# Performance work log

Hardware: AMD Instinct MI355X
Metric: run time of the kernel (lower is better)

The kernel has to match this reference:

```python
import jax, jax.numpy as jnp
import numpy as np

FEATURE_DIM = 768
NUM_HEADS = 16
HEAD_DIM = FEATURE_DIM // NUM_HEADS
SCALE = HEAD_DIM ** -0.5


def setup_inputs() -> dict:
    key = jax.random.key(0)
    ks = jax.random.split(key, 9)
    B, N, C = 4, 2048, FEATURE_DIM
    s = 0.02
    return {
        "x": jax.random.normal(ks[0], (B, N, C), dtype=jnp.float32),
        "wq": jax.random.normal(ks[1], (C, C), dtype=jnp.float32) * s,
        "bq": jax.random.normal(ks[2], (C,), dtype=jnp.float32) * s,
        "wk": jax.random.normal(ks[3], (C, C), dtype=jnp.float32) * s,
        "bk": jax.random.normal(ks[4], (C,), dtype=jnp.float32) * s,
        "wv": jax.random.normal(ks[5], (C, C), dtype=jnp.float32) * s,
        "bv": jax.random.normal(ks[6], (C,), dtype=jnp.float32) * s,
        "wo": jax.random.normal(ks[7], (C, C), dtype=jnp.float32) * s,
        "bo": jax.random.normal(ks[8], (C,), dtype=jnp.float32) * s,
    }


def reference(x, wq, bq, wk, bk, wv, bv, wo, bo):
    B, N, C = x.shape
    H, D = NUM_HEADS, HEAD_DIM
    # Linear layers use weight of shape (out, in): y = x @ W.T + b
    def proj(w, b):
        return (jnp.einsum("bnc,dc->bnd", x, w) + b).reshape(B, N, H, D).transpose(0, 2, 1, 3)
    q = proj(wq, bq)  # [B,H,N,D]
    k = proj(wk, bk)
    v = proj(wv, bv)
    attn = jnp.einsum("bhnd,bhmd->bhnm", q, k) * SCALE
    attn = jax.nn.softmax(attn, axis=-1)  # dropout = identity (eval mode)
    y = jnp.einsum("bhnm,bhmd->bhnd", attn, v).transpose(0, 2, 1, 3).reshape(B, N, C)
    y = y + x
    out = jnp.einsum("bnc,dc->bnd", y, wo) + bo
    out = out + y
    return out + x
```

## Files before the change

kernel.cpp:

```cpp
#include <hip/hip_runtime.h>
#include <hip/hip_bf16.h>

#define B_ 4
#define N_ 2048
#define C_ 768
#define H_ 16
#define D_ 48
#define SCALE_ 0.14433756729740643f
#define LOG2E_ 1.44269504088896f

using bf16 = __hip_bfloat16;
using bf16x8 = __attribute__((ext_vector_type(8))) short;
using f32x4  = __attribute__((ext_vector_type(4))) float;
using f32x16 = __attribute__((ext_vector_type(16))) float;

__device__ __forceinline__ unsigned short f2b(float f) {
  bf16 h = __float2bfloat16(f);
  return *reinterpret_cast<unsigned short*>(&h);
}
__device__ __forceinline__ unsigned int pack2(float lo, float hi) {
  return (unsigned int)f2b(lo) | ((unsigned int)f2b(hi) << 16);
}
__device__ __forceinline__ uint4 ld8f_cvt(const float* p) {
  float4 a = *reinterpret_cast<const float4*>(p);
  float4 b = *reinterpret_cast<const float4*>(p + 4);
  uint4 u;
  u.x = pack2(a.x, a.y); u.y = pack2(a.z, a.w);
  u.z = pack2(b.x, b.y); u.w = pack2(b.z, b.w);
  return u;
}
__device__ __forceinline__ void gload_lds16(const bf16* g, bf16* l) {
  __builtin_amdgcn_global_load_lds(
      (const __attribute__((address_space(1))) unsigned int*)g,
      (__attribute__((address_space(3))) unsigned int*)l, 16, 0, 0);
}

__global__ __launch_bounds__(256) void cvt_bf16(
    const float* __restrict__ x,  const float* __restrict__ wq,
    const float* __restrict__ wk, const float* __restrict__ wv,
    const float* __restrict__ wo,
    bf16* __restrict__ xb, bf16* __restrict__ wqkvb, bf16* __restrict__ wob)
{
  const int job = blockIdx.y;
  const float* src; bf16* dst; int n;
  if (job == 0)      { src = x;  dst = xb;              n = B_ * N_ * C_; }
  else if (job == 1) { src = wq; dst = wqkvb;           n = C_ * C_; }
  else if (job == 2) { src = wk; dst = wqkvb + C_ * C_; n = C_ * C_; }
  else if (job == 3) { src = wv; dst = wqkvb + 2 * C_ * C_; n = C_ * C_; }
  else               { src = wo; dst = wob;             n = C_ * C_; }
  const int stride = gridDim.x * 256 * 8;
  for (int i = (blockIdx.x * 256 + threadIdx.x) * 8; i < n; i += stride)
    *(uint4*)(dst + i) = ld8f_cvt(src + i);
}

__global__ __launch_bounds__(256) void gemm_qkv(
    const bf16* __restrict__ A, const bf16* __restrict__ Bw,
    const float* __restrict__ bq, const float* __restrict__ bk,
    const float* __restrict__ bv,
    bf16* __restrict__ Q, bf16* __restrict__ K, bf16* __restrict__ V)
{
  __shared__ __align__(16) bf16 As[128 * 64];
  __shared__ __align__(16) bf16 Bs[128 * 64];

  const int tid  = threadIdx.x;
  const int lane = tid & 63, wid = tid >> 6;
  const int wm = (wid >> 1) * 64, wn = (wid & 1) * 64;
  const int row0 = blockIdx.y * 128, col0 = blockIdx.x * 128;
  const int mb = lane & 15, g4 = lane >> 4;
  const int srow = lane >> 3;
  const int schunk = (lane & 7) ^ (srow & 7);

  f32x4 acc[4][4];
#pragma unroll
  for (int i = 0; i < 4; ++i)
#pragma unroll
    for (int j = 0; j < 4; ++j) acc[i][j] = (f32x4){0.f, 0.f, 0.f, 0.f};

  for (int k0 = 0; k0 < C_; k0 += 64) {
#pragma unroll
    for (int t = 0; t < 4; ++t) {
      const int rt = wid * 32 + t * 8;
      gload_lds16(A  + (size_t)(row0 + rt + srow) * C_ + k0 + schunk * 8,
                  As + rt * 64);
      gload_lds16(Bw + (size_t)(col0 + rt + srow) * C_ + k0 + schunk * 8,
                  Bs + rt * 64);
    }
    __syncthreads();
#pragma unroll
    for (int ks = 0; ks < 2; ++ks) {
      const int kchunk = ks * 4 + g4;
      bf16x8 af[4], bfr[4];
#pragma unroll
      for (int i = 0; i < 4; ++i) {
        const int row = wm + i * 16 + mb;
        af[i] = *(const bf16x8*)(As + row * 64 + (kchunk ^ (row & 7)) * 8);
      }
#pragma unroll
      for (int j = 0; j < 4; ++j) {
        const int col = wn + j * 16 + mb;
        bfr[j] = *(const bf16x8*)(Bs + col * 64 + (kchunk ^ (col & 7)) * 8);
      }
#pragma unroll
      for (int i = 0; i < 4; ++i)
#pragma unroll
        for (int j = 0; j < 4; ++j)
          acc[i][j] = __builtin_amdgcn_mfma_f32_16x16x32_bf16(af[i], bfr[j], acc[i][j], 0, 0, 0);
    }
    __syncthreads();
  }

  const int z = blockIdx.x / 6;
  const float* bias = (z == 0) ? bq : (z == 1) ? bk : bv;
  bf16* dst = (z == 0) ? Q : (z == 1) ? K : V;
  const float sc = (z == 0) ? (SCALE_ * LOG2E_) : 1.0f;
  const int crow = g4 * 4;
#pragma unroll
  for (int j = 0; j < 4; ++j) {
    const int oo = col0 - z * 768 + wn + j * 16 + mb;
    const int h = oo / D_, d = oo % D_;
    const float bb = bias[oo];
#pragma unroll
    for (int i = 0; i < 4; ++i) {
#pragma unroll
      for (int reg = 0; reg < 4; ++reg) {
        const int r = row0 + wm + i * 16 + crow + reg;
        const int b_ = r >> 11, n = r & (N_ - 1);
        dst[(((size_t)(b_ * H_ + h)) * N_ + n) * D_ + d] =
            __float2bfloat16((acc[i][j][reg] + bb) * sc);
      }
    }
  }
}

__global__ __launch_bounds__(256) void qkv_reshape(
    bf16* __restrict__ Q, bf16* __restrict__ K, bf16* __restrict__ V)
{
  __shared__ short T[64 * 50];
  const int bh = blockIdx.x;
  const int t0 = blockIdx.y * 64;
  const int tid = threadIdx.x;
  const size_t base = (size_t)bh * (N_ * D_) + (size_t)t0 * D_;
  bf16* bufs[3] = {Q, K, V};
#pragma unroll 1
  for (int wbuf = 0; wbuf < 3; ++wbuf) {
    bf16* P = bufs[wbuf] + base;
    for (int cc = tid; cc < 384; cc += 256) {
      const int r = cc / 6, ch = cc % 6;
      bf16x8 v8 = *(const bf16x8*)(P + r * D_ + ch * 8);
#pragma unroll
      for (int e = 0; e < 8; ++e) T[r * 50 + ch * 8 + e] = v8[e];
    }
    __syncthreads();
    if (wbuf < 2) {
      for (int w = tid; w < 384; w += 256) {
        const int sub = w / 192, rem = w % 192;
        const int kc = rem / 64, rem2 = rem % 64;
        const int g2 = rem2 >> 5, m5 = rem2 & 31;
        bf16x8 o;
#pragma unroll
        for (int e = 0; e < 8; ++e)
          o[e] = T[(sub * 32 + m5) * 50 + kc * 16 + g2 * 8 + e];
        *(bf16x8*)(P + w * 8) = o;
      }
    } else {
      for (int w = tid; w < 384; w += 256) {
        const int df = w / 128, rem = w % 128;
        const int hf = rem / 64, rem2 = rem % 64;
        const int g4 = rem2 >> 4, cx = rem2 & 15;
        bf16x8 o;
#pragma unroll
        for (int e = 0; e < 8; ++e)
          o[e] = T[(hf * 32 + g4 * 8 + e) * 50 + df * 16 + cx];
        *(bf16x8*)(P + w * 8) = o;
      }
    }
    __syncthreads();
  }
}

__global__ __launch_bounds__(256) void attn_mfma(
    const bf16* __restrict__ Qf, const bf16* __restrict__ Kf,
    const bf16* __restrict__ Vf, const float* __restrict__ x,
    bf16* __restrict__ Yb)
{
  __shared__ __align__(16) bf16 Ps[4 * 32 * 72];

  const int tid  = threadIdx.x;
  const int lane = tid & 63, wid = tid >> 6;
  const int m5 = lane & 31;
  const int g4 = lane >> 4, c = lane & 15;
  const int bh = blockIdx.x;
  const int b_ = bh >> 4, h = bh & 15;
  const int q0 = blockIdx.y * 128 + wid * 32;
  const size_t slab = (size_t)bh * (N_ * D_);
  bf16* Pw = Ps + wid * (32 * 72);

  bf16x8 qf[3];
  const int kgq = q0 >> 5;
#pragma unroll
  for (int kc = 0; kc < 3; ++kc)
    qf[kc] = *(const bf16x8*)(Qf + slab + (size_t)(((kgq * 3 + kc) * 64) + lane) * 8);

  const short one_bf = (short)0x3F80;
  const bf16x8 onesf = {one_bf, one_bf, one_bf, one_bf,
                        one_bf, one_bf, one_bf, one_bf};

  f32x4 Oacc[2][3];
  f32x4 Lacc[2];
#pragma unroll
  for (int s = 0; s < 2; ++s) {
    Lacc[s] = (f32x4){0.f, 0.f, 0.f, 0.f};
#pragma unroll
    for (int df = 0; df < 3; ++df) Oacc[s][df] = (f32x4){0.f, 0.f, 0.f, 0.f};
  }

  bf16x8 kf[2][2][3];
  auto loadK = [&](int kk0, int p) {
    const int kg = kk0 >> 5;
#pragma unroll
    for (int mt = 0; mt < 2; ++mt)
#pragma unroll
      for (int kc = 0; kc < 3; ++kc)
        kf[p][mt][kc] = *(const bf16x8*)(Kf + slab +
            (size_t)((((kg + mt) * 3 + kc) * 64) + lane) * 8);
  };
  auto body = [&](int k0c, int p) {
    const int kt = k0c >> 6;
    bf16x8 vf[3][2];
#pragma unroll
    for (int df = 0; df < 3; ++df)
#pragma unroll
      for (int hf = 0; hf < 2; ++hf)
        vf[df][hf] = *(const bf16x8*)(Vf + slab +
            (size_t)((((kt * 3 + df) * 2 + hf) * 64) + lane) * 8);
    f32x16 st[2];
#pragma unroll
    for (int mt = 0; mt < 2; ++mt) {
      f32x16 z;
#pragma unroll
      for (int r = 0; r < 16; ++r) z[r] = 0.f;
      st[mt] = __builtin_amdgcn_mfma_f32_32x32x16_bf16(kf[p][mt][0], qf[0], z, 0, 0, 0);
      st[mt] = __builtin_amdgcn_mfma_f32_32x32x16_bf16(kf[p][mt][1], qf[1], st[mt], 0, 0, 0);
      st[mt] = __builtin_amdgcn_mfma_f32_32x32x16_bf16(kf[p][mt][2], qf[2], st[mt], 0, 0, 0);
    }
#pragma unroll
    for (int mt = 0; mt < 2; ++mt)
#pragma unroll
      for (int r = 0; r < 16; ++r)
        st[mt][r] = __builtin_amdgcn_exp2f(st[mt][r]);
#pragma unroll
    for (int mt = 0; mt < 2; ++mt)
#pragma unroll
      for (int q = 0; q < 4; ++q) {
        uint2 w;
        w.x = pack2(st[mt][4 * q + 0], st[mt][4 * q + 1]);
        w.y = pack2(st[mt][4 * q + 2], st[mt][4 * q + 3]);
        *(uint2*)(Pw + m5 * 72 + mt * 32 + 8 * q + 4 * (lane >> 5)) = w;
      }
#pragma unroll
    for (int s = 0; s < 2; ++s) {
      bf16x8 pf[2];
#pragma unroll
      for (int hf = 0; hf < 2; ++hf)
        pf[hf] = *(const bf16x8*)(Pw + (s * 16 + c) * 72 + hf * 32 + 8 * g4);
#pragma unroll
      for (int df = 0; df < 3; ++df) {
        Oacc[s][df] = __builtin_amdgcn_mfma_f32_16x16x32_bf16(pf[0], vf[df][0], Oacc[s][df], 0, 0, 0);
        Oacc[s][df] = __builtin_amdgcn_mfma_f32_16x16x32_bf16(pf[1], vf[df][1], Oacc[s][df], 0, 0, 0);
      }
      Lacc[s] = __builtin_amdgcn_mfma_f32_16x16x32_bf16(pf[0], onesf, Lacc[s], 0, 0, 0);
      Lacc[s] = __builtin_amdgcn_mfma_f32_16x16x32_bf16(pf[1], onesf, Lacc[s], 0, 0, 0);
    }
  };

  loadK(0, 0);
  for (int k0 = 0; k0 < N_; k0 += 128) {
    loadK(k0 + 64, 1);
    body(k0, 0);
    if (k0 + 128 < N_) loadK(k0 + 128, 0);
    body(k0 + 64, 1);
  }

#pragma unroll
  for (int s = 0; s < 2; ++s) {
#pragma unroll
    for (int r = 0; r < 4; ++r) {
      const float inv = 1.f / Lacc[s][r];
      const int n = q0 + s * 16 + 4 * g4 + r;
      const size_t off = ((size_t)(b_ * N_ + n)) * C_ + h * D_ + c;
#pragma unroll
      for (int df = 0; df < 3; ++df)
        Yb[off + df * 16] =
            __float2bfloat16(Oacc[s][df][r] * inv + x[off + df * 16]);
    }
  }
}

__global__ __launch_bounds__(256) void gemm_out(
    const bf16* __restrict__ Yb, const bf16* __restrict__ Bw,
    const float* __restrict__ bo, const float* __restrict__ x,
    float* __restrict__ out)
{
  __shared__ __align__(16) bf16 As[128 * 64];
  __shared__ __align__(16) bf16 Bs[128 * 64];

  const int tid  = threadIdx.x;
  const int lane = tid & 63, wid = tid >> 6;
  const int wm = (wid >> 1) * 64, wn = (wid & 1) * 64;
  const int row0 = blockIdx.y * 128, col0 = blockIdx.x * 128;
  const int mb = lane & 15, g4 = lane >> 4;
  const int srow = lane >> 3;
  const int schunk = (lane & 7) ^ (srow & 7);

  f32x4 acc[4][4];
#pragma unroll
  for (int i = 0; i < 4; ++i)
#pragma unroll
    for (int j = 0; j < 4; ++j) acc[i][j] = (f32x4){0.f, 0.f, 0.f, 0.f};

  for (int k0 = 0; k0 < C_; k0 += 64) {
#pragma unroll
    for (int t = 0; t < 4; ++t) {
      const int rt = wid * 32 + t * 8;
      gload_lds16(Yb + (size_t)(row0 + rt + srow) * C_ + k0 + schunk * 8,
                  As + rt * 64);
      gload_lds16(Bw + (size_t)(col0 + rt + srow) * C_ + k0 + schunk * 8,
                  Bs + rt * 64);
    }
    __syncthreads();
#pragma unroll
    for (int ks = 0; ks < 2; ++ks) {
      const int kchunk = ks * 4 + g4;
      bf16x8 af[4], bfr[4];
#pragma unroll
      for (int i = 0; i < 4; ++i) {
        const int row = wm + i * 16 + mb;
        af[i] = *(const bf16x8*)(As + row * 64 + (kchunk ^ (row & 7)) * 8);
      }
#pragma unroll
      for (int j = 0; j < 4; ++j) {
        const int col = wn + j * 16 + mb;
        bfr[j] = *(const bf16x8*)(Bs + col * 64 + (kchunk ^ (col & 7)) * 8);
      }
#pragma unroll
      for (int i = 0; i < 4; ++i)
#pragma unroll
        for (int j = 0; j < 4; ++j)
          acc[i][j] = __builtin_amdgcn_mfma_f32_16x16x32_bf16(af[i], bfr[j], acc[i][j], 0, 0, 0);
    }
    __syncthreads();
  }

  const int crow = g4 * 4;
#pragma unroll
  for (int j = 0; j < 4; ++j) {
    const int o = col0 + wn + j * 16 + mb;
    const float bb = bo[o];
#pragma unroll
    for (int i = 0; i < 4; ++i) {
#pragma unroll
      for (int reg = 0; reg < 4; ++reg) {
        const int r = row0 + wm + i * 16 + crow + reg;
        const size_t off = (size_t)r * C_ + o;
        out[off] = acc[i][j][reg] + bb + __bfloat162float(Yb[off]) + x[off];
      }
    }
  }
}

extern "C" void kernel_launch(void* const* d_in, const int* in_sizes, int n_in,
                              void* d_out, int out_size, void* d_ws, size_t ws_size,
                              hipStream_t stream)
{
  const float* x  = (const float*)d_in[0];
  const float* wq = (const float*)d_in[1];
  const float* bq = (const float*)d_in[2];
  const float* wk = (const float*)d_in[3];
  const float* bk = (const float*)d_in[4];
  const float* wv = (const float*)d_in[5];
  const float* bv = (const float*)d_in[6];
  const float* wo = (const float*)d_in[7];
  const float* bo = (const float*)d_in[8];
  float* out = (float*)d_out;

  const size_t nEl = (size_t)B_ * N_ * C_;
  const size_t wEl = (size_t)C_ * C_;
  bf16* Q     = (bf16*)d_ws;
  bf16* K     = Q + nEl;
  bf16* V     = K + nEl;
  bf16* Yb    = V + nEl;
  bf16* xb    = Yb + nEl;
  bf16* wqkvb = xb + nEl;
  bf16* wob   = wqkvb + 3 * wEl;

  dim3 gcvt(768, 5);
  cvt_bf16<<<gcvt, dim3(256), 0, stream>>>(x, wq, wk, wv, wo, xb, wqkvb, wob);

  dim3 gqkv(18, 64);
  gemm_qkv<<<gqkv, dim3(256), 0, stream>>>(xb, wqkvb, bq, bk, bv, Q, K, V);

  dim3 grs(B_ * H_, N_ / 64);
  qkv_reshape<<<grs, dim3(256), 0, stream>>>(Q, K, V);

  dim3 gattn(B_ * H_, N_ / 128);
  attn_mfma<<<gattn, dim3(256), 0, stream>>>(Q, K, V, x, Yb);

  dim3 gout(6, 64);
  gemm_out<<<gout, dim3(256), 0, stream>>>(Yb, wob, bo, x, out);
}
```

Before: 272.0 us.

## Fuse QKV reshape into GEMM epilogue and software-pipeline attention loop

The separate qkv_reshape kernel is removed. The QKV GEMM now stages its output tile in shared memory and writes Q/K/V directly in the MFMA-fragment layout the attention kernel expects, which saves one kernel launch and a full read/write pass over Q, K and V. The attention loop is restructured so the QK^T/exp for tile t overlaps with the PV product for tile t-1, using double-buffered P tiles in LDS. A packed bf16 convert builtin is also used when available. The cost is doubled LDS for P and extra syncs in the GEMM epilogue.

Measured after the change: 297.2 us. 1.09x slower.

```diff
diff --git a/kernel.cpp b/kernel.cpp
--- a/kernel.cpp
+++ b/kernel.cpp
@@ -14,12 +14,24 @@
 using f32x4  = __attribute__((ext_vector_type(4))) float;
 using f32x16 = __attribute__((ext_vector_type(16))) float;
 
+#if defined(__has_builtin)
+#if __has_builtin(__builtin_amdgcn_cvt_pk_bf16_f32)
+#define HAS_PK_BF16 1
+#endif
+#endif
+
 __device__ __forceinline__ unsigned short f2b(float f) {
   bf16 h = __float2bfloat16(f);
   return *reinterpret_cast<unsigned short*>(&h);
 }
 __device__ __forceinline__ unsigned int pack2(float lo, float hi) {
+#ifdef HAS_PK_BF16
+  typedef __bf16 bf16x2v __attribute__((ext_vector_type(2)));
+  bf16x2v r = __builtin_amdgcn_cvt_pk_bf16_f32(lo, hi);
+  union { bf16x2v v; unsigned int u; } cv; cv.v = r; return cv.u;
+#else
   return (unsigned int)f2b(lo) | ((unsigned int)f2b(hi) << 16);
+#endif
 }
 __device__ __forceinline__ uint4 ld8f_cvt(const float* p) {
   float4 a = *reinterpret_cast<const float4*>(p);
@@ -59,8 +71,9 @@
     const float* __restrict__ bv,
     bf16* __restrict__ Q, bf16* __restrict__ K, bf16* __restrict__ V)
 {
-  __shared__ __align__(16) bf16 As[128 * 64];
-  __shared__ __align__(16) bf16 Bs[128 * 64];
+  __shared__ __align__(16) bf16 SH[2 * 128 * 64];
+  bf16* As = SH;
+  bf16* Bs = SH + 128 * 64;
 
   const int tid  = threadIdx.x;
   const int lane = tid & 63, wid = tid >> 6;
@@ -113,68 +126,75 @@
   const float* bias = (z == 0) ? bq : (z == 1) ? bk : bv;
   bf16* dst = (z == 0) ? Q : (z == 1) ? K : V;
   const float sc = (z == 0) ? (SCALE_ * LOG2E_) : 1.0f;
-  const int crow = g4 * 4;
-#pragma unroll
-  for (int j = 0; j < 4; ++j) {
-    const int oo = col0 - z * 768 + wn + j * 16 + mb;
-    const int h = oo / D_, d = oo % D_;
-    const float bb = bias[oo];
-#pragma unroll
-    for (int i = 0; i < 4; ++i) {
-#pragma unroll
-      for (int reg = 0; reg < 4; ++reg) {
-        const int r = row0 + wm + i * 16 + crow + reg;
-        const int b_ = r >> 11, n = r & (N_ - 1);
-        dst[(((size_t)(b_ * H_ + h)) * N_ + n) * D_ + d] =
-            __float2bfloat16((acc[i][j][reg] + bb) * sc);
-      }
-    }
-  }
-}
-
-__global__ __launch_bounds__(256) void qkv_reshape(
-    bf16* __restrict__ Q, bf16* __restrict__ K, bf16* __restrict__ V)
-{
-  __shared__ short T[64 * 50];
-  const int bh = blockIdx.x;
-  const int t0 = blockIdx.y * 64;
-  const int tid = threadIdx.x;
-  const size_t base = (size_t)bh * (N_ * D_) + (size_t)t0 * D_;
-  bf16* bufs[3] = {Q, K, V};
+  const int obase = (blockIdx.x % 6) * 128;
+  bf16* Cs = SH;
+
 #pragma unroll 1
-  for (int wbuf = 0; wbuf < 3; ++wbuf) {
-    bf16* P = bufs[wbuf] + base;
-    for (int cc = tid; cc < 384; cc += 256) {
-      const int r = cc / 6, ch = cc % 6;
-      bf16x8 v8 = *(const bf16x8*)(P + r * D_ + ch * 8);
-#pragma unroll
-      for (int e = 0; e < 8; ++e) T[r * 50 + ch * 8 + e] = v8[e];
-    }
-    __syncthreads();
-    if (wbuf < 2) {
-      for (int w = tid; w < 384; w += 256) {
-        const int sub = w / 192, rem = w % 192;
-        const int kc = rem / 64, rem2 = rem % 64;
-        const int g2 = rem2 >> 5, m5 = rem2 & 31;
-        bf16x8 o;
-#pragma unroll
-        for (int e = 0; e < 8; ++e)
-          o[e] = T[(sub * 32 + m5) * 50 + kc * 16 + g2 * 8 + e];
-        *(bf16x8*)(P + w * 8) = o;
+  for (int h2 = 0; h2 < 2; ++h2) {
+    __syncthreads();
+    if ((wid >> 1) == h2) {
+      if (z < 2) {
+#pragma unroll
+        for (int j = 0; j < 4; ++j) {
+          const int col = wn + j * 16 + mb;
+          const float bb = bias[obase + col];
+#pragma unroll
+          for (int i = 0; i < 4; ++i)
+#pragma unroll
+            for (int reg = 0; reg < 4; ++reg) {
+              const int rowL = i * 16 + 4 * g4 + reg;
+              Cs[rowL * 136 + col] =
+                  __float2bfloat16((acc[i][j][reg] + bb) * sc);
+            }
+        }
+      } else {
+#pragma unroll
+        for (int j = 0; j < 4; ++j) {
+          const int col = wn + j * 16 + mb;
+          const float bb = bias[obase + col];
+#pragma unroll
+          for (int i = 0; i < 4; ++i) {
+            uint2 wv;
+            wv.x = pack2(acc[i][j][0] + bb, acc[i][j][1] + bb);
+            wv.y = pack2(acc[i][j][2] + bb, acc[i][j][3] + bb);
+            *(uint2*)(Cs + col * 72 + i * 16 + 4 * g4) = wv;
+          }
+        }
+      }
+    }
+    __syncthreads();
+    const int rbase = row0 + h2 * 64;
+    const int bb_ = rbase >> 11;
+    const int nbase = rbase & (N_ - 1);
+    if (z < 2) {
+#pragma unroll
+      for (int t = 0; t < 4; ++t) {
+        const int w = t * 256 + tid;
+        const int m5w = w & 31, obw = (w >> 5) & 15, kgL = w >> 9;
+        const int m = (obase >> 3) + obw;
+        const int hh = m / 6, dd8 = m % 6;
+        const int n = nbase + kgL * 32 + m5w;
+        const size_t slab = (size_t)(bb_ * H_ + hh) * (N_ * D_);
+        const size_t chunk = (size_t)(((n >> 5) * 3 + (dd8 >> 1)) * 64
+                                      + (dd8 & 1) * 32 + m5w);
+        *(bf16x8*)(dst + slab + chunk * 8) =
+            *(const bf16x8*)(Cs + (kgL * 32 + m5w) * 136 + obw * 8);
       }
     } else {
-      for (int w = tid; w < 384; w += 256) {
-        const int df = w / 128, rem = w % 128;
-        const int hf = rem / 64, rem2 = rem % 64;
-        const int g4 = rem2 >> 4, cx = rem2 & 15;
-        bf16x8 o;
-#pragma unroll
-        for (int e = 0; e < 8; ++e)
-          o[e] = T[(hf * 32 + g4 * 8 + e) * 50 + df * 16 + cx];
-        *(bf16x8*)(P + w * 8) = o;
-      }
-    }
-    __syncthreads();
+#pragma unroll
+      for (int t = 0; t < 4; ++t) {
+        const int w = t * 256 + tid;
+        const int cw = w & 15, cb = (w >> 4) & 7, g4w = (w >> 7) & 3, hfw = w >> 9;
+        const int o = obase + cb * 16 + cw;
+        const int hh = o / 48, df = (o % 48) >> 4;
+        const int kt = nbase >> 6;
+        const size_t slab = (size_t)(bb_ * H_ + hh) * (N_ * D_);
+        const size_t chunk = (size_t)(((kt * 3 + df) * 2 + hfw) * 64
+                                      + g4w * 16 + cw);
+        *(bf16x8*)(dst + slab + chunk * 8) =
+            *(const bf16x8*)(Cs + (cb * 16 + cw) * 72 + hfw * 32 + g4w * 8);
+      }
+    }
   }
 }
 
@@ -183,23 +203,24 @@
     const bf16* __restrict__ Vf, const float* __restrict__ x,
     bf16* __restrict__ Yb)
 {
-  __shared__ __align__(16) bf16 Ps[4 * 32 * 72];
+  __shared__ __align__(16) bf16 Ps[4 * 2 * 32 * 72];
 
   const int tid  = threadIdx.x;
   const int lane = tid & 63, wid = tid >> 6;
-  const int m5 = lane & 31;
+  const int m5 = lane & 31, g2h = lane >> 5;
   const int g4 = lane >> 4, c = lane & 15;
   const int bh = blockIdx.x;
   const int b_ = bh >> 4, h = bh & 15;
   const int q0 = blockIdx.y * 128 + wid * 32;
   const size_t slab = (size_t)bh * (N_ * D_);
-  bf16* Pw = Ps + wid * (32 * 72);
+  bf16* Pw0 = Ps + wid * 2 * (32 * 72);
+  bf16* Pw1 = Pw0 + 32 * 72;
 
   bf16x8 qf[3];
   const int kgq = q0 >> 5;
 #pragma unroll
   for (int kc = 0; kc < 3; ++kc)
-    qf[kc] = *(const bf16x8*)(Qf + slab + (size_t)(((kgq * 3 + kc) * 64) + lane) * 8);
+    qf[kc] = *(const bf16x8*)(Qf + slab + (size_t)((kgq * 3 + kc) * 64 + lane) * 8);
 
   const short one_bf = (short)0x3F80;
   const bf16x8 onesf = {one_bf, one_bf, one_bf, one_bf,
@@ -215,54 +236,51 @@
   }
 
   bf16x8 kf[2][2][3];
-  auto loadK = [&](int kk0, int p) {
-    const int kg = kk0 >> 5;
+  bf16x8 vf[3][2];
+
+  auto loadK = [&](int t, int p) {
 #pragma unroll
     for (int mt = 0; mt < 2; ++mt)
 #pragma unroll
       for (int kc = 0; kc < 3; ++kc)
         kf[p][mt][kc] = *(const bf16x8*)(Kf + slab +
-            (size_t)((((kg + mt) * 3 + kc) * 64) + lane) * 8);
+            (size_t)(((2 * t + mt) * 3 + kc) * 64 + lane) * 8);
   };
-  auto body = [&](int k0c, int p) {
-    const int kt = k0c >> 6;
-    bf16x8 vf[3][2];
+  auto loadV = [&](int t) {
 #pragma unroll
     for (int df = 0; df < 3; ++df)
 #pragma unroll
       for (int hf = 0; hf < 2; ++hf)
         vf[df][hf] = *(const bf16x8*)(Vf + slab +
-            (size_t)((((kt * 3 + df) * 2 + hf) * 64) + lane) * 8);
-    f32x16 st[2];
+            (size_t)(((t * 3 + df) * 2 + hf) * 64 + lane) * 8);
+  };
+  auto SexpPack = [&](int p, bf16* pw) {
 #pragma unroll
     for (int mt = 0; mt < 2; ++mt) {
-      f32x16 z;
-#pragma unroll
-      for (int r = 0; r < 16; ++r) z[r] = 0.f;
-      st[mt] = __builtin_amdgcn_mfma_f32_32x32x16_bf16(kf[p][mt][0], qf[0], z, 0, 0, 0);
-      st[mt] = __builtin_amdgcn_mfma_f32_32x32x16_bf16(kf[p][mt][1], qf[1], st[mt], 0, 0, 0);
-      st[mt] = __builtin_amdgcn_mfma_f32_32x32x16_bf16(kf[p][mt][2], qf[2], st[mt], 0, 0, 0);
-    }
-#pragma unroll
-    for (int mt = 0; mt < 2; ++mt)
-#pragma unroll
-      for (int r = 0; r < 16; ++r)
-        st[mt][r] = __builtin_amdgcn_exp2f(st[mt][r]);
-#pragma unroll
-    for (int mt = 0; mt < 2; ++mt)
+      f32x16 st;
+#pragma unroll
+      for (int r = 0; r < 16; ++r) st[r] = 0.f;
+      st = __builtin_amdgcn_mfma_f32_32x32x16_bf16(kf[p][mt][0], qf[0], st, 0, 0, 0);
+      st = __builtin_amdgcn_mfma_f32_32x32x16_bf16(kf[p][mt][1], qf[1], st, 0, 0, 0);
+      st = __builtin_amdgcn_mfma_f32_32x32x16_bf16(kf[p][mt][2], qf[2], st, 0, 0, 0);
+#pragma unroll
+      for (int r = 0; r < 16; ++r) st[r] = __builtin_amdgcn_exp2f(st[r]);
 #pragma unroll
       for (int q = 0; q < 4; ++q) {
         uint2 w;
-        w.x = pack2(st[mt][4 * q + 0], st[mt][4 * q + 1]);
-        w.y = pack2(st[mt][4 * q + 2], st[mt][4 * q + 3]);
-        *(uint2*)(Pw + m5 * 72 + mt * 32 + 8 * q + 4 * (lane >> 5)) = w;
-      }
+        w.x = pack2(st[4 * q + 0], st[4 * q + 1]);
+        w.y = pack2(st[4 * q + 2], st[4 * q + 3]);
+        *(uint2*)(pw + m5 * 72 + mt * 32 + 8 * q + 4 * g2h) = w;
+      }
+    }
+  };
+  auto PV = [&](const bf16* pw) {
 #pragma unroll
     for (int s = 0; s < 2; ++s) {
       bf16x8 pf[2];
 #pragma unroll
       for (int hf = 0; hf < 2; ++hf)
-        pf[hf] = *(const bf16x8*)(Pw + (s * 16 + c) * 72 + hf * 32 + 8 * g4);
+        pf[hf] = *(const bf16x8*)(pw + (s * 16 + c) * 72 + hf * 32 + 8 * g4);
 #pragma unroll
       for (int df = 0; df < 3; ++df) {
         Oacc[s][df] = __builtin_amdgcn_mfma_f32_16x16x32_bf16(pf[0], vf[df][0], Oacc[s][df], 0, 0, 0);
@@ -274,12 +292,21 @@
   };
 
   loadK(0, 0);
-  for (int k0 = 0; k0 < N_; k0 += 128) {
-    loadK(k0 + 64, 1);
-    body(k0, 0);
-    if (k0 + 128 < N_) loadK(k0 + 128, 0);
-    body(k0 + 64, 1);
-  }
+  loadK(1, 1);
+  loadV(0);
+  SexpPack(0, Pw0);
+
+#pragma unroll 2
+  for (int t = 1; t < 32; ++t) {
+    const int p = t & 1;
+    if (t + 1 < 32) loadK(t + 1, (t + 1) & 1);
+    bf16* pwCur  = p ? Pw1 : Pw0;
+    bf16* pwPrev = p ? Pw0 : Pw1;
+    SexpPack(p, pwCur);
+    PV(pwPrev);
+    loadV(t);
+  }
+  PV(Pw1);
 
 #pragma unroll
   for (int s = 0; s < 2; ++s) {
@@ -399,9 +426,6 @@
   dim3 gqkv(18, 64);
   gemm_qkv<<<gqkv, dim3(256), 0, stream>>>(xb, wqkvb, bq, bk, bv, Q, K, V);
 
-  dim3 grs(B_ * H_, N_ / 64);
-  qkv_reshape<<<grs, dim3(256), 0, stream>>>(Q, K, V);
-
   dim3 gattn(B_ * H_, N_ / 128);
   attn_mfma<<<gattn, dim3(256), 0, stream>>>(Q, K, V, x, Yb);
 
```

## Split attention key range across warps and merge partial sums in LDS

Applied to the files above, without the earlier changes.

Each attention block now covers 64 queries instead of 128, and its four warps form two query groups times two key halves. Each warp processes half of the keys, and the partial O and L accumulators are combined through shared memory before the final normalization. This doubles the number of blocks to fill the GPU better and shortens each warp's serial key loop, at the cost of two barriers, extra LDS traffic, and each K/V tile being loaded by twice as many blocks. It also switches bf16 packing to the hardware packed-convert builtin when it is available, and simplifies the QKV output column index.

After: 467.3 us. 71.8% more time.

```diff
diff --git a/kernel.cpp b/kernel.cpp
--- a/kernel.cpp
+++ b/kernel.cpp
@@ -14,12 +14,24 @@
 using f32x4  = __attribute__((ext_vector_type(4))) float;
 using f32x16 = __attribute__((ext_vector_type(16))) float;
 
+#if defined(__has_builtin)
+#if __has_builtin(__builtin_amdgcn_cvt_pk_bf16_f32)
+#define HAS_PK_BF16 1
+#endif
+#endif
+
 __device__ __forceinline__ unsigned short f2b(float f) {
   bf16 h = __float2bfloat16(f);
   return *reinterpret_cast<unsigned short*>(&h);
 }
 __device__ __forceinline__ unsigned int pack2(float lo, float hi) {
+#ifdef HAS_PK_BF16
+  typedef __bf16 bf16x2v __attribute__((ext_vector_type(2)));
+  bf16x2v r = __builtin_amdgcn_cvt_pk_bf16_f32(lo, hi);
+  union { bf16x2v v; unsigned int u; } cv; cv.v = r; return cv.u;
+#else
   return (unsigned int)f2b(lo) | ((unsigned int)f2b(hi) << 16);
+#endif
 }
 __device__ __forceinline__ uint4 ld8f_cvt(const float* p) {
   float4 a = *reinterpret_cast<const float4*>(p);
@@ -113,10 +125,11 @@
   const float* bias = (z == 0) ? bq : (z == 1) ? bk : bv;
   bf16* dst = (z == 0) ? Q : (z == 1) ? K : V;
   const float sc = (z == 0) ? (SCALE_ * LOG2E_) : 1.0f;
+  const int obase = (blockIdx.x % 6) * 128;
   const int crow = g4 * 4;
 #pragma unroll
   for (int j = 0; j < 4; ++j) {
-    const int oo = col0 - z * 768 + wn + j * 16 + mb;
+    const int oo = obase + wn + j * 16 + mb;
     const int h = oo / D_, d = oo % D_;
     const float bb = bias[oo];
 #pragma unroll
@@ -184,14 +197,18 @@
     bf16* __restrict__ Yb)
 {
   __shared__ __align__(16) bf16 Ps[4 * 32 * 72];
+  __shared__ float Cb[2 * 32 * 49];
+  __shared__ float Lb[2 * 32];
 
   const int tid  = threadIdx.x;
   const int lane = tid & 63, wid = tid >> 6;
-  const int m5 = lane & 31;
+  const int m5 = lane & 31, g2h = lane >> 5;
   const int g4 = lane >> 4, c = lane & 15;
   const int bh = blockIdx.x;
   const int b_ = bh >> 4, h = bh & 15;
-  const int q0 = blockIdx.y * 128 + wid * 32;
+  const int qw = wid & 1, kh = wid >> 1;
+  const int q0 = blockIdx.y * 64 + qw * 32;
+  const int tbase = kh * 16;
   const size_t slab = (size_t)bh * (N_ * D_);
   bf16* Pw = Ps + wid * (32 * 72);
 
@@ -199,7 +216,7 @@
   const int kgq = q0 >> 5;
 #pragma unroll
   for (int kc = 0; kc < 3; ++kc)
-    qf[kc] = *(const bf16x8*)(Qf + slab + (size_t)(((kgq * 3 + kc) * 64) + lane) * 8);
+    qf[kc] = *(const bf16x8*)(Qf + slab + (size_t)((kgq * 3 + kc) * 64 + lane) * 8);
 
   const short one_bf = (short)0x3F80;
   const bf16x8 onesf = {one_bf, one_bf, one_bf, one_bf,
@@ -215,48 +232,49 @@
   }
 
   bf16x8 kf[2][2][3];
-  auto loadK = [&](int kk0, int p) {
-    const int kg = kk0 >> 5;
+  bf16x8 vf[3][2];
+
+  auto loadK = [&](int t, int p) {
 #pragma unroll
     for (int mt = 0; mt < 2; ++mt)
 #pragma unroll
       for (int kc = 0; kc < 3; ++kc)
         kf[p][mt][kc] = *(const bf16x8*)(Kf + slab +
-            (size_t)((((kg + mt) * 3 + kc) * 64) + lane) * 8);
+            (size_t)(((2 * t + mt) * 3 + kc) * 64 + lane) * 8);
   };
-  auto body = [&](int k0c, int p) {
-    const int kt = k0c >> 6;
-    bf16x8 vf[3][2];
+  auto loadV = [&](int t) {
 #pragma unroll
     for (int df = 0; df < 3; ++df)
 #pragma unroll
       for (int hf = 0; hf < 2; ++hf)
         vf[df][hf] = *(const bf16x8*)(Vf + slab +
-            (size_t)((((kt * 3 + df) * 2 + hf) * 64) + lane) * 8);
-    f32x16 st[2];
+            (size_t)(((t * 3 + df) * 2 + hf) * 64 + lane) * 8);
+  };
+
+  loadK(tbase, 0);
+#pragma unroll 1
+  for (int i = 0; i < 16; ++i) {
+    const int p = i & 1;
+    if (i + 1 < 16) loadK(tbase + i + 1, (i + 1) & 1);
+    loadV(tbase + i);
 #pragma unroll
     for (int mt = 0; mt < 2; ++mt) {
-      f32x16 z;
-#pragma unroll
-      for (int r = 0; r < 16; ++r) z[r] = 0.f;
-      st[mt] = __builtin_amdgcn_mfma_f32_32x32x16_bf16(kf[p][mt][0], qf[0], z, 0, 0, 0);
-      st[mt] = __builtin_amdgcn_mfma_f32_32x32x16_bf16(kf[p][mt][1], qf[1], st[mt], 0, 0, 0);
-      st[mt] = __builtin_amdgcn_mfma_f32_32x32x16_bf16(kf[p][mt][2], qf[2], st[mt], 0, 0, 0);
-    }
-#pragma unroll
-    for (int mt = 0; mt < 2; ++mt)
-#pragma unroll
-      for (int r = 0; r < 16; ++r)
-        st[mt][r] = __builtin_amdgcn_exp2f(st[mt][r]);
-#pragma unroll
-    for (int mt = 0; mt < 2; ++mt)
+      f32x16 st;
+#pragma unroll
+      for (int r = 0; r < 16; ++r) st[r] = 0.f;
+      st = __builtin_amdgcn_mfma_f32_32x32x16_bf16(kf[p][mt][0], qf[0], st, 0, 0, 0);
+      st = __builtin_amdgcn_mfma_f32_32x32x16_bf16(kf[p][mt][1], qf[1], st, 0, 0, 0);
+      st = __builtin_amdgcn_mfma_f32_32x32x16_bf16(kf[p][mt][2], qf[2], st, 0, 0, 0);
+#pragma unroll
+      for (int r = 0; r < 16; ++r) st[r] = __builtin_amdgcn_exp2f(st[r]);
 #pragma unroll
       for (int q = 0; q < 4; ++q) {
         uint2 w;
-        w.x = pack2(st[mt][4 * q + 0], st[mt][4 * q + 1]);
-        w.y = pack2(st[mt][4 * q + 2], st[mt][4 * q + 3]);
-        *(uint2*)(Pw + m5 * 72 + mt * 32 + 8 * q + 4 * (lane >> 5)) = w;
-      }
+        w.x = pack2(st[4 * q + 0], st[4 * q + 1]);
+        w.y = pack2(st[4 * q + 2], st[4 * q + 3]);
+        *(uint2*)(Pw + m5 * 72 + mt * 32 + 8 * q + 4 * g2h) = w;
+      }
+    }
 #pragma unroll
     for (int s = 0; s < 2; ++s) {
       bf16x8 pf[2];
@@ -271,28 +289,37 @@
       Lacc[s] = __builtin_amdgcn_mfma_f32_16x16x32_bf16(pf[0], onesf, Lacc[s], 0, 0, 0);
       Lacc[s] = __builtin_amdgcn_mfma_f32_16x16x32_bf16(pf[1], onesf, Lacc[s], 0, 0, 0);
     }
-  };
-
-  loadK(0, 0);
-  for (int k0 = 0; k0 < N_; k0 += 128) {
-    loadK(k0 + 64, 1);
-    body(k0, 0);
-    if (k0 + 128 < N_) loadK(k0 + 128, 0);
-    body(k0 + 64, 1);
-  }
-
-#pragma unroll
-  for (int s = 0; s < 2; ++s) {
-#pragma unroll
-    for (int r = 0; r < 4; ++r) {
-      const float inv = 1.f / Lacc[s][r];
-      const int n = q0 + s * 16 + 4 * g4 + r;
-      const size_t off = ((size_t)(b_ * N_ + n)) * C_ + h * D_ + c;
-#pragma unroll
-      for (int df = 0; df < 3; ++df)
-        Yb[off + df * 16] =
-            __float2bfloat16(Oacc[s][df][r] * inv + x[off + df * 16]);
-    }
+  }
+
+  __syncthreads();
+  if (kh == 1) {
+#pragma unroll
+    for (int s = 0; s < 2; ++s)
+#pragma unroll
+      for (int r = 0; r < 4; ++r) {
+        const int row = s * 16 + 4 * g4 + r;
+#pragma unroll
+        for (int df = 0; df < 3; ++df)
+          Cb[(qw * 32 + row) * 49 + df * 16 + c] = Oacc[s][df][r];
+        if (c == 0) Lb[qw * 32 + row] = Lacc[s][r];
+      }
+  }
+  __syncthreads();
+  if (kh == 0) {
+#pragma unroll
+    for (int s = 0; s < 2; ++s)
+#pragma unroll
+      for (int r = 0; r < 4; ++r) {
+        const int row = s * 16 + 4 * g4 + r;
+        const float inv = 1.f / (Lacc[s][r] + Lb[qw * 32 + row]);
+        const int n = q0 + row;
+        const size_t off = ((size_t)(b_ * N_ + n)) * C_ + h * D_ + c;
+#pragma unroll
+        for (int df = 0; df < 3; ++df) {
+          const float o = Oacc[s][df][r] + Cb[(qw * 32 + row) * 49 + df * 16 + c];
+          Yb[off + df * 16] = __float2bfloat16(o * inv + x[off + df * 16]);
+        }
+      }
   }
 }
 
@@ -402,7 +429,7 @@
   dim3 grs(B_ * H_, N_ / 64);
   qkv_reshape<<<grs, dim3(256), 0, stream>>>(Q, K, V);
 
-  dim3 gattn(B_ * H_, N_ / 128);
+  dim3 gattn(B_ * H_, N_ / 64);
   attn_mfma<<<gattn, dim3(256), 0, stream>>>(Q, K, V, x, Yb);
 
   dim3 gout(6, 64);
```
